# Performance work log

Hardware: AMD Instinct MI355X
Metric: run time of the kernel (lower is better)

## Reference

```python
import jax, jax.numpy as jnp
import numpy as np

EPS_LN = 1e-5
EPS_SUM = 1e-5


def setup_inputs() -> dict:
    key = jax.random.key(0)
    ks = jax.random.split(key, 6)
    B, T, F, D = 8, 1024, 512, 64
    x = jax.random.normal(ks[0], (B, T, F), dtype=jnp.float32)
    state = jnp.zeros((B, 1, D * D), dtype=jnp.float32)
    s = 1.0 / np.sqrt(F)
    Wk = jax.random.uniform(ks[1], (F, D), jnp.float32, -s, s)
    Wq = jax.random.uniform(ks[2], (F, D), jnp.float32, -s, s)
    Wv = jax.random.uniform(ks[3], (F, D), jnp.float32, -s, s)
    gamma = jnp.ones((F,), jnp.float32)
    beta = jnp.zeros((F,), jnp.float32)
    return {"x": x, "state": state, "Wk": Wk, "Wq": Wq, "Wv": Wv,
            "gamma": gamma, "beta": beta}


def _layernorm(x, gamma, beta):
    mu = jnp.mean(x, axis=-1, keepdims=True)
    var = jnp.mean(jnp.square(x - mu), axis=-1, keepdims=True)
    return (x - mu) * jax.lax.rsqrt(var + EPS_LN) * gamma + beta


def reference(x, state, Wk, Wq, Wv, gamma, beta):
    B, T, F = x.shape
    D = Wk.shape[1]
    xn = _layernorm(x, gamma, beta)
    K = jax.nn.relu(xn @ Wk)            # [B,T,D]
    Q = jax.nn.relu(xn @ Wq)
    V = xn @ Wv
    # sum normalization (paper)
    K = K / (EPS_SUM + jnp.sum(K, axis=-1, keepdims=True))
    Q = Q / (EPS_SUM + jnp.sum(Q, axis=-1, keepdims=True))
    # outer-product fast weights per step: kv[b,t,i,j] = V[b,t,i] * K[b,t,j]
    kv = jnp.einsum('bti,btj->btij', V, K)        # [B,T,D,D]
    # 'sum' aggregator: running (cumulative) sum seeded by the initial state
    state_seq = state.reshape(B, 1, D, D) + jnp.cumsum(kv, axis=1)  # [B,T,D,D]
    y = jnp.einsum('btij,bti->btj', state_seq, Q)  # [B,T,D]
    return (y, state_seq)
```

## Files before the change

kernel.cpp:

```cpp
#include <hip/hip_runtime.h>

#define BB 8
#define TT 1024
#define FF 512
#define DD 64
#define LCH 16
#define CCH (TT / LCH)
#define SEG 8
#define NSEG (CCH / SEG)
#define EE (DD * DD)

__device__ __forceinline__ float wave_sum64(float v) {
  #pragma unroll
  for (int m = 32; m >= 1; m >>= 1) v += __shfl_xor(v, m, 64);
  return v;
}

__global__ __launch_bounds__(256) void lnprojcs_k(
    const float* __restrict__ x,
    const float* __restrict__ gamma, const float* __restrict__ beta,
    const float* __restrict__ Wk, const float* __restrict__ Wq,
    const float* __restrict__ Wv,
    float* __restrict__ Ko, float* __restrict__ Qo, float* __restrict__ Vo,
    float* __restrict__ S) {
  __shared__ float smem[9216];
  float* lx   = smem;
  float* part = smem;
  float* lk   = smem + 6144;
  float* lv   = smem + 7168;

  const int tid = threadIdx.x;
  const int wv = tid >> 6, lane = tid & 63;
  const int bc = blockIdx.x;
  const size_t row0 = (size_t)bc * LCH;

  {
    const float4* xg = (const float4*)(x + row0 * FF);
    float4* lx4 = (float4*)lx;
    #pragma unroll
    for (int i = 0; i < 8; ++i)
      lx4[tid + 256 * i] = xg[tid + 256 * i];
  }
  __syncthreads();

  {
    float g[8], bt[8];
    #pragma unroll
    for (int k = 0; k < 8; ++k) {
      g[k]  = gamma[lane + 64 * k];
      bt[k] = beta[lane + 64 * k];
    }
    #pragma unroll
    for (int rr = 0; rr < 4; ++rr) {
      int r = wv * 4 + rr;
      float v[8];
      float s = 0.f, ss = 0.f;
      #pragma unroll
      for (int k = 0; k < 8; ++k) {
        v[k] = lx[r * FF + lane + 64 * k];
        s += v[k]; ss += v[k] * v[k];
      }
      s = wave_sum64(s); ss = wave_sum64(ss);
      float m = s * (1.f / FF);
      float var = ss * (1.f / FF) - m * m;
      float rs = rsqrtf(var + 1e-5f);
      #pragma unroll
      for (int k = 0; k < 8; ++k)
        lx[r * FF + lane + 64 * k] = (v[k] - m) * rs * g[k] + bt[k];
    }
  }
  __syncthreads();

  float acc[LCH][3];
  #pragma unroll
  for (int r = 0; r < LCH; ++r)
    #pragma unroll
    for (int p = 0; p < 3; ++p) acc[r][p] = 0.f;

  const int fbase = wv * (FF / 4);
  #pragma unroll 2
  for (int f0 = fbase; f0 < fbase + FF / 4; f0 += 4) {
    float wk0 = Wk[(f0 + 0) * DD + lane], wk1 = Wk[(f0 + 1) * DD + lane];
    float wk2 = Wk[(f0 + 2) * DD + lane], wk3 = Wk[(f0 + 3) * DD + lane];
    float wq0 = Wq[(f0 + 0) * DD + lane], wq1 = Wq[(f0 + 1) * DD + lane];
    float wq2 = Wq[(f0 + 2) * DD + lane], wq3 = Wq[(f0 + 3) * DD + lane];
    float wv0 = Wv[(f0 + 0) * DD + lane], wv1 = Wv[(f0 + 1) * DD + lane];
    float wv2 = Wv[(f0 + 2) * DD + lane], wv3 = Wv[(f0 + 3) * DD + lane];
    #pragma unroll
    for (int r = 0; r < LCH; ++r) {
      float4 xv = *(const float4*)&lx[r * FF + f0];
      acc[r][0] += (xv.x * wk0 + xv.y * wk1) + (xv.z * wk2 + xv.w * wk3);
      acc[r][1] += (xv.x * wq0 + xv.y * wq1) + (xv.z * wq2 + xv.w * wq3);
      acc[r][2] += (xv.x * wv0 + xv.y * wv1) + (xv.z * wv2 + xv.w * wv3);
    }
  }
  __syncthreads();

  #pragma unroll
  for (int h = 0; h < 2; ++h) {
    #pragma unroll
    for (int r = 0; r < 8; ++r)
      #pragma unroll
      for (int p = 0; p < 3; ++p)
        part[((wv * 8 + r) * 3 + p) * DD + lane] = acc[h * 8 + r][p];
    __syncthreads();
    #pragma unroll
    for (int i = 0; i < 6; ++i) {
      int pid = wv * 6 + i;
      int r = pid / 3, p = pid - r * 3;
      float val = part[((0 * 8 + r) * 3 + p) * DD + lane]
                + part[((1 * 8 + r) * 3 + p) * DD + lane]
                + part[((2 * 8 + r) * 3 + p) * DD + lane]
                + part[((3 * 8 + r) * 3 + p) * DD + lane];
      if (p < 2) {
        val = fmaxf(val, 0.f);
        float sm = wave_sum64(val);
        val = val / (1e-5f + sm);
      }
      int rg = h * 8 + r;
      float* outp = (p == 0) ? Ko : (p == 1) ? Qo : Vo;
      outp[(row0 + rg) * DD + lane] = val;
      if (p == 0)      lk[rg * DD + lane] = val;
      else if (p == 2) lv[rg * DD + lane] = val;
    }
    __syncthreads();
  }

  {
    const int j = lane, s0 = wv << 4;
    float a2[16];
    #pragma unroll
    for (int ii = 0; ii < 16; ++ii) a2[ii] = 0.f;
    #pragma unroll
    for (int t = 0; t < LCH; ++t) {
      float kj = lk[t * DD + j];
      #pragma unroll
      for (int ii = 0; ii < 16; ++ii) a2[ii] += lv[t * DD + s0 + ii] * kj;
    }
    float* Sp = S + (size_t)bc * EE;
    #pragma unroll
    for (int ii = 0; ii < 16; ++ii) Sp[(s0 + ii) * DD + j] = a2[ii];
  }
}

__global__ __launch_bounds__(256) void segsum_k(const float* __restrict__ S,
                                                float* __restrict__ Z) {
  int blk = blockIdx.x;
  int b = blk >> 7;
  int seg = (blk >> 4) & 7;
  int e = ((blk & 15) << 8) + threadIdx.x;
  const float* Sb = S + ((size_t)(b * CCH + seg * SEG)) * EE + e;
  float sv[SEG];
  #pragma unroll
  for (int c = 0; c < SEG; ++c) sv[c] = Sb[(size_t)c * EE];
  float acc = 0.f;
  #pragma unroll
  for (int c = 0; c < SEG; ++c) acc += sv[c];
  Z[((size_t)(b * NSEG + seg)) * EE + e] = acc;
}

__global__ __launch_bounds__(256) void scan_k(const float* __restrict__ Kx,
                     const float* __restrict__ Qx, const float* __restrict__ Vx,
                     const float* __restrict__ S, const float* __restrict__ Z,
                     const float* __restrict__ st0,
                     float* __restrict__ y, float* __restrict__ sout) {
  int bc = blockIdx.x, tid = threadIdx.x;
  int wv = tid >> 6, j = tid & 63;
  int i0 = wv * 16;
  int b = bc >> 6, c = bc & (CCH - 1);
  int seg = c >> 3, cin = c & 7;
  __shared__ float yp[4][LCH][DD];

  float run[16];
  {
    const float* s0p = st0 + (size_t)b * EE;
    #pragma unroll
    for (int ii = 0; ii < 16; ++ii) run[ii] = s0p[(i0 + ii) * DD + j];
    const float* Zb = Z + (size_t)b * NSEG * EE;
    for (int s = 0; s < seg; ++s) {
      const float* Zs = Zb + (size_t)s * EE;
      #pragma unroll
      for (int ii = 0; ii < 16; ++ii) run[ii] += Zs[(i0 + ii) * DD + j];
    }
    const float* Sb = S + ((size_t)(b * CCH + seg * SEG)) * EE;
    for (int cc = 0; cc < cin; ++cc) {
      const float* Sc = Sb + (size_t)cc * EE;
      #pragma unroll
      for (int ii = 0; ii < 16; ++ii) run[ii] += Sc[(i0 + ii) * DD + j];
    }
  }

  const float* Kb = Kx + (size_t)bc * LCH * DD;
  const float* Vb = Vx + (size_t)bc * LCH * DD;
  const float* Qb = Qx + (size_t)bc * LCH * DD;
  float kreg[LCH];
  #pragma unroll
  for (int t = 0; t < LCH; ++t) kreg[t] = Kb[t * DD + j];
  float* so = sout + (size_t)bc * LCH * EE + (size_t)i0 * DD + j;
  for (int t = 0; t < LCH; ++t) {
    const float* Vt = Vb + t * DD + i0;
    const float* Qt = Qb + t * DD + i0;
    float kj = kreg[t];
    float y0 = 0.f, y1 = 0.f, y2 = 0.f, y3 = 0.f;
    float* sot = so + (size_t)t * EE;
    #pragma unroll
    for (int ii = 0; ii < 16; ii += 4) {
      run[ii]     += Vt[ii]     * kj; sot[(ii)     * DD] = run[ii];     y0 += run[ii]     * Qt[ii];
      run[ii + 1] += Vt[ii + 1] * kj; sot[(ii + 1) * DD] = run[ii + 1]; y1 += run[ii + 1] * Qt[ii + 1];
      run[ii + 2] += Vt[ii + 2] * kj; sot[(ii + 2) * DD] = run[ii + 2]; y2 += run[ii + 2] * Qt[ii + 2];
      run[ii + 3] += Vt[ii + 3] * kj; sot[(ii + 3) * DD] = run[ii + 3]; y3 += run[ii + 3] * Qt[ii + 3];
    }
    yp[wv][t][j] = (y0 + y1) + (y2 + y3);
  }
  __syncthreads();
  float* yo = y + (size_t)bc * LCH * DD;
  #pragma unroll
  for (int tt = 0; tt < LCH / 4; ++tt) {
    int t = wv * (LCH / 4) + tt;
    yo[t * DD + j] = (yp[0][t][j] + yp[1][t][j]) + (yp[2][t][j] + yp[3][t][j]);
  }
}

extern "C" void kernel_launch(void* const* d_in, const int* in_sizes, int n_in,
                              void* d_out, int out_size, void* d_ws, size_t ws_size,
                              hipStream_t stream) {
  const float* x     = (const float*)d_in[0];
  const float* st0   = (const float*)d_in[1];
  const float* Wk    = (const float*)d_in[2];
  const float* Wq    = (const float*)d_in[3];
  const float* Wv    = (const float*)d_in[4];
  const float* gamma = (const float*)d_in[5];
  const float* beta  = (const float*)d_in[6];

  float* out  = (float*)d_out;
  float* yout = out;
  float* sseq = out + (size_t)BB * TT * DD;

  float* ws = (float*)d_ws;
  float* Ko = ws;
  float* Qo = Ko + (size_t)BB * TT * DD;
  float* Vo = Qo + (size_t)BB * TT * DD;
  float* S  = Vo + (size_t)BB * TT * DD;
  float* Z  = S  + (size_t)BB * CCH * EE;

  lnprojcs_k<<<BB * CCH, 256, 0, stream>>>(x, gamma, beta, Wk, Wq, Wv, Ko, Qo, Vo, S);
  segsum_k  <<<BB * NSEG * 16, 256, 0, stream>>>(S, Z);
  scan_k    <<<BB * CCH, 256, 0, stream>>>(Ko, Qo, Vo, S, Z, st0, yout, sseq);
}
```

Baseline: 215.5 us.

## Use split-bf16 MFMA for projections and precompute per-chunk scan prefixes

The LN+projection GEMM moves from scalar FP32 FMAs to MFMA bf16 16x16x32 instructions. Both operands are split into high and low bf16 halves and combined with four MFMAs to keep near-FP32 accuracy. Weights are pre-split and re-laid out by a new kernel on every call. A new segscan kernel writes each chunk's starting state, so scan_k no longer re-accumulates up to fourteen prefix matrices per block, at the cost of an extra full-state pass and one more launch.

```diff
diff --git a/kernel.cpp b/kernel.cpp
--- a/kernel.cpp
+++ b/kernel.cpp
@@ -9,25 +9,60 @@
 #define SEG 8
 #define NSEG (CCH / SEG)
 #define EE (DD * DD)
+#define NCT 12
+#define AST 520
+#define CST 196
+
+typedef short short8 __attribute__((ext_vector_type(8)));
+typedef float f32x4 __attribute__((ext_vector_type(4)));
 
 __device__ __forceinline__ float wave_sum64(float v) {
   #pragma unroll
   for (int m = 32; m >= 1; m >>= 1) v += __shfl_xor(v, m, 64);
   return v;
+}
+
+__device__ __forceinline__ unsigned short f2bf(float f) {
+  unsigned int u = __float_as_uint(f);
+  u += 0x7FFFu + ((u >> 16) & 1u);
+  return (unsigned short)(u >> 16);
+}
+__device__ __forceinline__ float bf2f(unsigned short h) {
+  return __uint_as_float(((unsigned int)h) << 16);
+}
+
+__global__ __launch_bounds__(64) void wprep_k(
+    const float* __restrict__ Wk, const float* __restrict__ Wq,
+    const float* __restrict__ Wv,
+    unsigned short* __restrict__ Wh, unsigned short* __restrict__ Wl) {
+  int blk = blockIdx.x;
+  int ct = blk >> 4, kk = blk & 15;
+  int lane = threadIdx.x;
+  int p = ct >> 2;
+  const float* Wp = (p == 0) ? Wk : (p == 1) ? Wq : Wv;
+  int d = ((ct & 3) << 4) + (lane & 15);
+  int k0 = (kk << 5) + ((lane >> 4) << 3);
+  size_t o = ((size_t)blk * 64 + lane) * 8;
+  #pragma unroll
+  for (int j = 0; j < 8; ++j) {
+    float w = Wp[(size_t)(k0 + j) * DD + d];
+    unsigned short h = f2bf(w);
+    float rem = w - bf2f(h);
+    Wh[o + j] = h;
+    Wl[o + j] = f2bf(rem);
+  }
 }
 
 __global__ __launch_bounds__(256) void lnprojcs_k(
     const float* __restrict__ x,
     const float* __restrict__ gamma, const float* __restrict__ beta,
-    const float* __restrict__ Wk, const float* __restrict__ Wq,
-    const float* __restrict__ Wv,
+    const unsigned short* __restrict__ Wh, const unsigned short* __restrict__ Wl,
     float* __restrict__ Ko, float* __restrict__ Qo, float* __restrict__ Vo,
     float* __restrict__ S) {
-  __shared__ float smem[9216];
-  float* lx   = smem;
-  float* part = smem;
-  float* lk   = smem + 6144;
-  float* lv   = smem + 7168;
+  __shared__ __align__(16) char smem[2 * LCH * AST * 2];
+  unsigned short* lxh = (unsigned short*)smem;
+  unsigned short* lxl = lxh + LCH * AST;
+  float* lkqv = (float*)smem;
 
   const int tid = threadIdx.x;
   const int wv = tid >> 6, lane = tid & 63;
@@ -35,15 +70,6 @@
   const size_t row0 = (size_t)bc * LCH;
 
   {
-    const float4* xg = (const float4*)(x + row0 * FF);
-    float4* lx4 = (float4*)lx;
-    #pragma unroll
-    for (int i = 0; i < 8; ++i)
-      lx4[tid + 256 * i] = xg[tid + 256 * i];
-  }
-  __syncthreads();
-
-  {
     float g[8], bt[8];
     #pragma unroll
     for (int k = 0; k < 8; ++k) {
@@ -53,11 +79,12 @@
     #pragma unroll
     for (int rr = 0; rr < 4; ++rr) {
       int r = wv * 4 + rr;
+      const float* xr = x + (row0 + r) * FF;
       float v[8];
       float s = 0.f, ss = 0.f;
       #pragma unroll
       for (int k = 0; k < 8; ++k) {
-        v[k] = lx[r * FF + lane + 64 * k];
+        v[k] = xr[lane + 64 * k];
         s += v[k]; ss += v[k] * v[k];
       }
       s = wave_sum64(s); ss = wave_sum64(ss);
@@ -65,81 +92,94 @@
       float var = ss * (1.f / FF) - m * m;
       float rs = rsqrtf(var + 1e-5f);
       #pragma unroll
-      for (int k = 0; k < 8; ++k)
-        lx[r * FF + lane + 64 * k] = (v[k] - m) * rs * g[k] + bt[k];
-    }
-  }
-  __syncthreads();
-
-  float acc[LCH][3];
-  #pragma unroll
-  for (int r = 0; r < LCH; ++r)
-    #pragma unroll
-    for (int p = 0; p < 3; ++p) acc[r][p] = 0.f;
-
-  const int fbase = wv * (FF / 4);
-  #pragma unroll 2
-  for (int f0 = fbase; f0 < fbase + FF / 4; f0 += 4) {
-    float wk0 = Wk[(f0 + 0) * DD + lane], wk1 = Wk[(f0 + 1) * DD + lane];
-    float wk2 = Wk[(f0 + 2) * DD + lane], wk3 = Wk[(f0 + 3) * DD + lane];
-    float wq0 = Wq[(f0 + 0) * DD + lane], wq1 = Wq[(f0 + 1) * DD + lane];
-    float wq2 = Wq[(f0 + 2) * DD + lane], wq3 = Wq[(f0 + 3) * DD + lane];
-    float wv0 = Wv[(f0 + 0) * DD + lane], wv1 = Wv[(f0 + 1) * DD + lane];
-    float wv2 = Wv[(f0 + 2) * DD + lane], wv3 = Wv[(f0 + 3) * DD + lane];
-    #pragma unroll
-    for (int r = 0; r < LCH; ++r) {
-      float4 xv = *(const float4*)&lx[r * FF + f0];
-      acc[r][0] += (xv.x * wk0 + xv.y * wk1) + (xv.z * wk2 + xv.w * wk3);
-      acc[r][1] += (xv.x * wq0 + xv.y * wq1) + (xv.z * wq2 + xv.w * wq3);
-      acc[r][2] += (xv.x * wv0 + xv.y * wv1) + (xv.z * wv2 + xv.w * wv3);
-    }
-  }
-  __syncthreads();
-
-  #pragma unroll
-  for (int h = 0; h < 2; ++h) {
-    #pragma unroll
-    for (int r = 0; r < 8; ++r)
+      for (int k = 0; k < 8; ++k) {
+        float xv = (v[k] - m) * rs * g[k] + bt[k];
+        unsigned short h = f2bf(xv);
+        float rem = xv - bf2f(h);
+        lxh[r * AST + lane + 64 * k] = h;
+        lxl[r * AST + lane + 64 * k] = f2bf(rem);
+      }
+    }
+  }
+  __syncthreads();
+
+  f32x4 acc0 = {0.f, 0.f, 0.f, 0.f};
+  f32x4 acc1 = {0.f, 0.f, 0.f, 0.f};
+  f32x4 acc2 = {0.f, 0.f, 0.f, 0.f};
+  {
+    const int arow = lane & 15, agrp = lane >> 4;
+    const unsigned short* abase = lxh + arow * AST + agrp * 8;
+    const size_t wbase = (((size_t)(wv * 3) * 16) * 64 + lane) * 8;
+    for (int kk = 0; kk < 16; ++kk) {
+      const unsigned short* ap = abase + kk * 32;
+      short8 ah = *(const short8*)ap;
+      short8 al = *(const short8*)(ap + LCH * AST);
+      size_t wo = wbase + (size_t)kk * 64 * 8;
+      short8 bh0 = *(const short8*)(Wh + wo);
+      short8 bl0 = *(const short8*)(Wl + wo);
+      short8 bh1 = *(const short8*)(Wh + wo + 8192);
+      short8 bl1 = *(const short8*)(Wl + wo + 8192);
+      short8 bh2 = *(const short8*)(Wh + wo + 16384);
+      short8 bl2 = *(const short8*)(Wl + wo + 16384);
+      acc0 = __builtin_amdgcn_mfma_f32_16x16x32_bf16(ah, bh0, acc0, 0, 0, 0);
+      acc0 = __builtin_amdgcn_mfma_f32_16x16x32_bf16(ah, bl0, acc0, 0, 0, 0);
+      acc0 = __builtin_amdgcn_mfma_f32_16x16x32_bf16(al, bh0, acc0, 0, 0, 0);
+      acc0 = __builtin_amdgcn_mfma_f32_16x16x32_bf16(al, bl0, acc0, 0, 0, 0);
+      acc1 = __builtin_amdgcn_mfma_f32_16x16x32_bf16(ah, bh1, acc1, 0, 0, 0);
+      acc1 = __builtin_amdgcn_mfma_f32_16x16x32_bf16(ah, bl1, acc1, 0, 0, 0);
+      acc1 = __builtin_amdgcn_mfma_f32_16x16x32_bf16(al, bh1, acc1, 0, 0, 0);
+      acc1 = __builtin_amdgcn_mfma_f32_16x16x32_bf16(al, bl1, acc1, 0, 0, 0);
+      acc2 = __builtin_amdgcn_mfma_f32_16x16x32_bf16(ah, bh2, acc2, 0, 0, 0);
+      acc2 = __builtin_amdgcn_mfma_f32_16x16x32_bf16(ah, bl2, acc2, 0, 0, 0);
+      acc2 = __builtin_amdgcn_mfma_f32_16x16x32_bf16(al, bh2, acc2, 0, 0, 0);
+      acc2 = __builtin_amdgcn_mfma_f32_16x16x32_bf16(al, bl2, acc2, 0, 0, 0);
+    }
+  }
+  __syncthreads();
+
+  {
+    const int ccol = lane & 15, crow0 = (lane >> 4) << 2;
+    const int n0 = (wv * 3) << 4;
+    #pragma unroll
+    for (int reg = 0; reg < 4; ++reg) {
+      lkqv[(crow0 + reg) * CST + n0 +  0 + ccol] = acc0[reg];
+      lkqv[(crow0 + reg) * CST + n0 + 16 + ccol] = acc1[reg];
+      lkqv[(crow0 + reg) * CST + n0 + 32 + ccol] = acc2[reg];
+    }
+  }
+  __syncthreads();
+
+  #pragma unroll
+  for (int i = 0; i < 12; ++i) {
+    int pid = wv * 12 + i;
+    int r = pid / 3, p = pid - r * 3;
+    float val = lkqv[r * CST + p * 64 + lane];
+    if (p < 2) {
+      val = fmaxf(val, 0.f);
+      float sm = wave_sum64(val);
+      val = val / (1e-5f + sm);
+    }
+    float* outp = (p == 0) ? Ko : (p == 1) ? Qo : Vo;
+    outp[(row0 + r) * DD + lane] = val;
+    lkqv[r * CST + p * 64 + lane] = val;
+  }
+  __syncthreads();
+
+  {
+    const int j = lane, s0i = wv << 4;
+    float a2[16];
+    #pragma unroll
+    for (int ii = 0; ii < 16; ++ii) a2[ii] = 0.f;
+    #pragma unroll
+    for (int t = 0; t < LCH; ++t) {
+      float kj = lkqv[t * CST + j];
       #pragma unroll
-      for (int p = 0; p < 3; ++p)
-        part[((wv * 8 + r) * 3 + p) * DD + lane] = acc[h * 8 + r][p];
-    __syncthreads();
-    #pragma unroll
-    for (int i = 0; i < 6; ++i) {
-      int pid = wv * 6 + i;
-      int r = pid / 3, p = pid - r * 3;
-      float val = part[((0 * 8 + r) * 3 + p) * DD + lane]
-                + part[((1 * 8 + r) * 3 + p) * DD + lane]
-                + part[((2 * 8 + r) * 3 + p) * DD + lane]
-                + part[((3 * 8 + r) * 3 + p) * DD + lane];
-      if (p < 2) {
-        val = fmaxf(val, 0.f);
-        float sm = wave_sum64(val);
-        val = val / (1e-5f + sm);
-      }
-      int rg = h * 8 + r;
-      float* outp = (p == 0) ? Ko : (p == 1) ? Qo : Vo;
-      outp[(row0 + rg) * DD + lane] = val;
-      if (p == 0)      lk[rg * DD + lane] = val;
-      else if (p == 2) lv[rg * DD + lane] = val;
-    }
-    __syncthreads();
-  }
-
-  {
-    const int j = lane, s0 = wv << 4;
-    float a2[16];
-    #pragma unroll
-    for (int ii = 0; ii < 16; ++ii) a2[ii] = 0.f;
-    #pragma unroll
-    for (int t = 0; t < LCH; ++t) {
-      float kj = lk[t * DD + j];
-      #pragma unroll
-      for (int ii = 0; ii < 16; ++ii) a2[ii] += lv[t * DD + s0 + ii] * kj;
+      for (int ii = 0; ii < 16; ++ii)
+        a2[ii] += lkqv[t * CST + 128 + s0i + ii] * kj;
     }
     float* Sp = S + (size_t)bc * EE;
     #pragma unroll
-    for (int ii = 0; ii < 16; ++ii) Sp[(s0 + ii) * DD + j] = a2[ii];
+    for (int ii = 0; ii < 16; ++ii) Sp[(s0i + ii) * DD + j] = a2[ii];
   }
 }
 
@@ -159,37 +199,45 @@
   Z[((size_t)(b * NSEG + seg)) * EE + e] = acc;
 }
 
+__global__ __launch_bounds__(256) void segscan_k(const float* __restrict__ S,
+                                                 const float* __restrict__ Z,
+                                                 const float* __restrict__ st0,
+                                                 float* __restrict__ P) {
+  int blk = blockIdx.x;
+  int b = blk >> 7;
+  int seg = (blk >> 4) & 7;
+  int e = ((blk & 15) << 8) + threadIdx.x;
+  float run = st0[(size_t)b * EE + e];
+  const float* Zb = Z + (size_t)b * NSEG * EE + e;
+  float zv[NSEG - 1];
+  #pragma unroll
+  for (int s = 0; s < NSEG - 1; ++s) zv[s] = Zb[(size_t)s * EE];
+  #pragma unroll
+  for (int s = 0; s < NSEG - 1; ++s) if (s < seg) run += zv[s];
+  const float* Sb = S + ((size_t)(b * CCH + seg * SEG)) * EE + e;
+  float* Pb = P + ((size_t)(b * CCH + seg * SEG)) * EE + e;
+  float sv[SEG];
+  #pragma unroll
+  for (int c = 0; c < SEG; ++c) sv[c] = Sb[(size_t)c * EE];
+  #pragma unroll
+  for (int c = 0; c < SEG; ++c) {
+    Pb[(size_t)c * EE] = run;
+    run += sv[c];
+  }
+}
+
 __global__ __launch_bounds__(256) void scan_k(const float* __restrict__ Kx,
                      const float* __restrict__ Qx, const float* __restrict__ Vx,
-                     const float* __restrict__ S, const float* __restrict__ Z,
-                     const float* __restrict__ st0,
+                     const float* __restrict__ P,
                      float* __restrict__ y, float* __restrict__ sout) {
   int bc = blockIdx.x, tid = threadIdx.x;
   int wv = tid >> 6, j = tid & 63;
   int i0 = wv * 16;
-  int b = bc >> 6, c = bc & (CCH - 1);
-  int seg = c >> 3, cin = c & 7;
   __shared__ float yp[4][LCH][DD];
-
-  float run[16];
-  {
-    const float* s0p = st0 + (size_t)b * EE;
-    #pragma unroll
-    for (int ii = 0; ii < 16; ++ii) run[ii] = s0p[(i0 + ii) * DD + j];
-    const float* Zb = Z + (size_t)b * NSEG * EE;
-    for (int s = 0; s < seg; ++s) {
-      const float* Zs = Zb + (size_t)s * EE;
-      #pragma unroll
-      for (int ii = 0; ii < 16; ++ii) run[ii] += Zs[(i0 + ii) * DD + j];
-    }
-    const float* Sb = S + ((size_t)(b * CCH + seg * SEG)) * EE;
-    for (int cc = 0; cc < cin; ++cc) {
-      const float* Sc = Sb + (size_t)cc * EE;
-      #pragma unroll
-      for (int ii = 0; ii < 16; ++ii) run[ii] += Sc[(i0 + ii) * DD + j];
-    }
-  }
-
+  float Sr[16];
+  const float* Pp = P + (size_t)bc * EE;
+  #pragma unroll
+  for (int ii = 0; ii < 16; ++ii) Sr[ii] = Pp[(i0 + ii) * DD + j];
   const float* Kb = Kx + (size_t)bc * LCH * DD;
   const float* Vb = Vx + (size_t)bc * LCH * DD;
   const float* Qb = Qx + (size_t)bc * LCH * DD;
@@ -205,10 +253,10 @@
     float* sot = so + (size_t)t * EE;
     #pragma unroll
     for (int ii = 0; ii < 16; ii += 4) {
-      run[ii]     += Vt[ii]     * kj; sot[(ii)     * DD] = run[ii];     y0 += run[ii]     * Qt[ii];
-      run[ii + 1] += Vt[ii + 1] * kj; sot[(ii + 1) * DD] = run[ii + 1]; y1 += run[ii + 1] * Qt[ii + 1];
-      run[ii + 2] += Vt[ii + 2] * kj; sot[(ii + 2) * DD] = run[ii + 2]; y2 += run[ii + 2] * Qt[ii + 2];
-      run[ii + 3] += Vt[ii + 3] * kj; sot[(ii + 3) * DD] = run[ii + 3]; y3 += run[ii + 3] * Qt[ii + 3];
+      Sr[ii]     += Vt[ii]     * kj; sot[(ii)     * DD] = Sr[ii];     y0 += Sr[ii]     * Qt[ii];
+      Sr[ii + 1] += Vt[ii + 1] * kj; sot[(ii + 1) * DD] = Sr[ii + 1]; y1 += Sr[ii + 1] * Qt[ii + 1];
+      Sr[ii + 2] += Vt[ii + 2] * kj; sot[(ii + 2) * DD] = Sr[ii + 2]; y2 += Sr[ii + 2] * Qt[ii + 2];
+      Sr[ii + 3] += Vt[ii + 3] * kj; sot[(ii + 3) * DD] = Sr[ii + 3]; y3 += Sr[ii + 3] * Qt[ii + 3];
     }
     yp[wv][t][j] = (y0 + y1) + (y2 + y3);
   }
@@ -241,9 +289,14 @@
   float* Qo = Ko + (size_t)BB * TT * DD;
   float* Vo = Qo + (size_t)BB * TT * DD;
   float* S  = Vo + (size_t)BB * TT * DD;
-  float* Z  = S  + (size_t)BB * CCH * EE;
-
-  lnprojcs_k<<<BB * CCH, 256, 0, stream>>>(x, gamma, beta, Wk, Wq, Wv, Ko, Qo, Vo, S);
+  float* P  = S  + (size_t)BB * CCH * EE;
+  float* Z  = P  + (size_t)BB * CCH * EE;
+  unsigned short* Wh = (unsigned short*)(Z + (size_t)BB * NSEG * EE);
+  unsigned short* Wl = Wh + (size_t)NCT * 16 * 64 * 8;
+
+  wprep_k   <<<NCT * 16, 64, 0, stream>>>(Wk, Wq, Wv, Wh, Wl);
+  lnprojcs_k<<<BB * CCH, 256, 0, stream>>>(x, gamma, beta, Wh, Wl, Ko, Qo, Vo, S);
   segsum_k  <<<BB * NSEG * 16, 256, 0, stream>>>(S, Z);
-  scan_k    <<<BB * CCH, 256, 0, stream>>>(Ko, Qo, Vo, S, Z, st0, yout, sseq);
-}
+  segscan_k <<<BB * NSEG * 16, 256, 0, stream>>>(S, Z, st0, P);
+  scan_k    <<<BB * CCH, 256, 0, stream>>>(Ko, Qo, Vo, P, yout, sseq);
+}
```

New measurement: 187.9 us (median of 2 runs). -12.8%, faster.
